# Performance work log

Measured on AMD Instinct MI355X. Metric: run time of the kernel, lower is better.

Reference implementation:

```python
import jax, jax.numpy as jnp
import numpy as np

# CODABlocks (codomain attention) with per_channel_attention=True:
# token_codimension = head_codimension = 1, scale = 2, n_modes = [32, 32],
# mixer_modes = [16, 16], temperature = 1.0, instance_norm (affine) everywhere.
N_HEADS = 16
TEMPERATURE = 1.0
EPS = 1e-5

def _gelu(z):
    return jax.nn.gelu(z, approximate=False)  # matches torch F.gelu default (erf)

def instance_norm(x, g, b):
    # x: (B, C, H, W); normalize over spatial dims per (sample, channel), affine.
    mu = jnp.mean(x, axis=(-2, -1), keepdims=True)
    var = jnp.var(x, axis=(-2, -1), keepdims=True)
    return (x - mu) * jax.lax.rsqrt(var + EPS) * g[:, None, None] + b[:, None, None]

def conv1x1(x, w, b):
    return jnp.einsum('bihw,io->bohw', x, w) + b[None, :, None, None]

def fourier_resample(x, out_shape):
    # FFT-based spatial resampling (mode truncation / zero-pad), norm='forward'.
    if tuple(x.shape[-2:]) == tuple(out_shape):
        return x
    Ho, Wo = out_shape
    xft = jnp.fft.rfftn(x, axes=(-2, -1), norm='forward')
    out = jnp.zeros(x.shape[:-2] + (Ho, Wo // 2 + 1), dtype=xft.dtype)
    hk = min(x.shape[-2], Ho) // 2
    wk = min(xft.shape[-1], Wo // 2 + 1)
    out = out.at[..., :hk, :wk].set(xft[..., :hk, :wk])
    out = out.at[..., -hk:, :wk].set(xft[..., -hk:, :wk])
    return jnp.fft.irfftn(out, s=out_shape, axes=(-2, -1), norm='forward')

def spectral_conv(x, w, out_shape):
    # Truncated-mode spectral convolution (dense weights, equiv. to tucker rank=1.0).
    # w: (Cin, Cout, 2*mh, mw, 2) -> complex weight on kept Fourier modes.
    wc = w[..., 0] + 1j * w[..., 1]
    mh = wc.shape[2] // 2
    mw = wc.shape[3]
    Ho, Wo = out_shape
    xft = jnp.fft.rfftn(x, axes=(-2, -1), norm='forward')   # (B, Cin, H, W//2+1)
    top = jnp.einsum('bihw,iohw->bohw', xft[:, :, :mh, :mw], wc[:, :, :mh])
    bot = jnp.einsum('bihw,iohw->bohw', xft[:, :, -mh:, :mw], wc[:, :, mh:])
    out_ft = jnp.zeros((x.shape[0], wc.shape[1], Ho, Wo // 2 + 1), dtype=xft.dtype)
    out_ft = out_ft.at[:, :, :mh, :mw].set(top)
    out_ft = out_ft.at[:, :, -mh:, :mw].set(bot)
    return jnp.fft.irfftn(out_ft, s=out_shape, axes=(-2, -1), norm='forward')

def fno_layer(x, spec_w, skip_w, skip_b, out_shape, norm=None, act=None):
    # One FNOBlocks layer: spectral conv + (resampled) linear skip, optional norm/act.
    xs = fourier_resample(conv1x1(x, skip_w, skip_b), out_shape)
    xf = spectral_conv(x, spec_w, out_shape)
    if norm is not None:
        xf = instance_norm(xf, *norm)
    y = xf + xs
    return act(y) if act is not None else y

def codano_forward(x, key_w, key_skip_w, key_skip_b, query_w, query_skip_w, query_skip_b, value_w, value_skip_w, value_skip_b, proj_w, proj_skip_w, proj_skip_b, norm1_g, norm1_b, attn_norm_g, attn_norm_b, norm2_g, norm2_b, mixer_w1, mixer_skip_w1, mixer_skip_b1, mixer_norm_g1, mixer_norm_b1, mixer_w2, mixer_skip_w2, mixer_skip_b2, mixer_norm_g2, mixer_norm_b2, mixer_out_g, mixer_out_b):
    b, t, H, W = x.shape   # token codim d = 1 -> channel dim == number of tokens
    tokens = x.reshape(b * t, 1, H, W)
    tokens_norm = instance_norm(tokens, norm1_g, norm1_b)
    Hs, Ws = H // 2, W // 2   # K, Q downsampled by scale = 2
    k = fno_layer(tokens_norm, key_w, key_skip_w, key_skip_b, (Hs, Ws))
    q = fno_layer(tokens_norm, query_w, query_skip_w, query_skip_b, (Hs, Ws))
    v = fno_layer(tokens_norm, value_w, value_skip_w, value_skip_b, (H, W))

    def heads_flat(z):
        hh, ww = z.shape[-2:]
        # (b*t, n_heads*d, h, w) -> (b, heads, t, d*h*w), d = 1
        return z.reshape(b, t, N_HEADS, hh * ww).transpose(0, 2, 1, 3)

    kf, qf, vf = heads_flat(k), heads_flat(q), heads_flat(v)
    scale = jnp.sqrt(jnp.asarray(kf.shape[-1], jnp.float32)) * TEMPERATURE
    dprod = jax.nn.softmax(jnp.einsum('bhtd,bhsd->bhts', qf, kf) / scale, axis=-1)
    attn = jnp.einsum('bhts,bhsd->bhtd', dprod, vf)      # (b, heads, t, H*W)
    attn = attn.transpose(0, 2, 1, 3).reshape(b * t, N_HEADS, H, W)
    # multi-head projection back to token codimension (n_heads -> 1)
    attn = fno_layer(attn, proj_w, proj_skip_w, proj_skip_b, (H, W))
    attn = instance_norm(attn + tokens, attn_norm_g, attn_norm_b)
    # permutation-equivariant mixer: 2 FNO layers shared across all tokens
    m = instance_norm(attn, norm2_g, norm2_b)
    m = fno_layer(m, mixer_w1, mixer_skip_w1, mixer_skip_b1, (H, W), norm=(mixer_norm_g1, mixer_norm_b1), act=_gelu)
    m = fno_layer(m, mixer_w2, mixer_skip_w2, mixer_skip_b2, (H, W), norm=(mixer_norm_g2, mixer_norm_b2))
    out = instance_norm(m, mixer_out_g, mixer_out_b) + attn
    return out.reshape(b, t, H, W)

def setup_inputs():
    key = jax.random.key(0)
    ks = list(jax.random.split(key, 32))
    f32 = jnp.float32
    def W_(k, shape, s=0.02):
        return (s * jax.random.normal(k, shape)).astype(f32)
    B, T, H, Wd = 4, 32, 128, 128
    mh_s, mw_s = 16, 9    # mixer_modes [16,16]: 2*(16//2) rows, 16//2+1 rfft cols
    mh_f, mw_f = 32, 17   # n_modes [32,32]
    return {
        'x': jax.random.normal(ks[0], (B, T, H, Wd), dtype=f32),
        'key_w': W_(ks[1], (1, N_HEADS, mh_s, mw_s, 2)),
        'key_skip_w': W_(ks[2], (1, N_HEADS), 0.5),
        'key_skip_b': W_(ks[3], (N_HEADS,)),
        'query_w': W_(ks[4], (1, N_HEADS, mh_s, mw_s, 2)),
        'query_skip_w': W_(ks[5], (1, N_HEADS), 0.5),
        'query_skip_b': W_(ks[6], (N_HEADS,)),
        'value_w': W_(ks[7], (1, N_HEADS, mh_s, mw_s, 2)),
        'value_skip_w': W_(ks[8], (1, N_HEADS), 0.5),
        'value_skip_b': W_(ks[9], (N_HEADS,)),
        'proj_w': W_(ks[10], (N_HEADS, 1, mh_f, mw_f, 2)),
        'proj_skip_w': W_(ks[11], (N_HEADS, 1), 0.25),
        'proj_skip_b': W_(ks[12], (1,)),
        'norm1_g': jnp.ones((1,), f32), 'norm1_b': jnp.zeros((1,), f32),
        'attn_norm_g': jnp.ones((1,), f32), 'attn_norm_b': jnp.zeros((1,), f32),
        'norm2_g': jnp.ones((1,), f32), 'norm2_b': jnp.zeros((1,), f32),
        'mixer_w1': W_(ks[13], (1, 1, mh_f, mw_f, 2)),
        'mixer_skip_w1': W_(ks[14], (1, 1), 0.5),
        'mixer_skip_b1': W_(ks[15], (1,)),
        'mixer_norm_g1': jnp.ones((1,), f32), 'mixer_norm_b1': jnp.zeros((1,), f32),
        'mixer_w2': W_(ks[16], (1, 1, mh_f, mw_f, 2)),
        'mixer_skip_w2': W_(ks[17], (1, 1), 0.5),
        'mixer_skip_b2': W_(ks[18], (1,)),
        'mixer_norm_g2': jnp.ones((1,), f32), 'mixer_norm_b2': jnp.zeros((1,), f32),
        'mixer_out_g': jnp.ones((1,), f32), 'mixer_out_b': jnp.zeros((1,), f32),
    }

def reference(x, key_w, key_skip_w, key_skip_b, query_w, query_skip_w, query_skip_b, value_w, value_skip_w, value_skip_b, proj_w, proj_skip_w, proj_skip_b, norm1_g, norm1_b, attn_norm_g, attn_norm_b, norm2_g, norm2_b, mixer_w1, mixer_skip_w1, mixer_skip_b1, mixer_norm_g1, mixer_norm_b1, mixer_w2, mixer_skip_w2, mixer_skip_b2, mixer_norm_g2, mixer_norm_b2, mixer_out_g, mixer_out_b):
    return codano_forward(x, key_w, key_skip_w, key_skip_b, query_w, query_skip_w, query_skip_b, value_w, value_skip_w, value_skip_b, proj_w, proj_skip_w, proj_skip_b, norm1_g, norm1_b, attn_norm_g, attn_norm_b, norm2_g, norm2_b, mixer_w1, mixer_skip_w1, mixer_skip_b1, mixer_norm_g1, mixer_norm_b1, mixer_w2, mixer_skip_w2, mixer_skip_b2, mixer_norm_g2, mixer_norm_b2, mixer_out_g, mixer_out_b)
```

## Files before the change

kernel.cpp:

```cpp
#include <hip/hip_runtime.h>
#include <cmath>

#define PI_F 3.14159265358979323846f
#define NTOK 128
#define NPIX 16384
#define NHEADS 16

__device__ __forceinline__ void block_reduce2(float& a, float& b){
  __shared__ float sa[4], sb[4];
  __syncthreads();
  for (int o=32;o>0;o>>=1){ a += __shfl_down(a,o); b += __shfl_down(b,o); }
  int w = threadIdx.x>>6, l = threadIdx.x&63;
  if (l==0){ sa[w]=a; sb[w]=b; }
  __syncthreads();
  a = sa[0]+sa[1]+sa[2]+sa[3];
  b = sb[0]+sb[1]+sb[2]+sb[3];
}

__device__ __forceinline__ float block_reduce1(float a){
  __shared__ float sa[4];
  __syncthreads();
  for (int o=32;o>0;o>>=1) a += __shfl_down(a,o);
  int w = threadIdx.x>>6, l = threadIdx.x&63;
  if (l==0) sa[w]=a;
  __syncthreads();
  return sa[0]+sa[1]+sa[2]+sa[3];
}

__device__ __forceinline__ float gelu_f(float y){
  return 0.5f*y*(1.f + erff(y*0.70710678118f));
}

__device__ __forceinline__ void affine_from(const float* __restrict__ ps, float g, float bb, int t,
                                            float& a, float& b0){
  float sum=0.f,sq=0.f;
  #pragma unroll
  for (int s=0;s<8;s++){ const float* p=ps+((size_t)t*8+s)*2; sum+=p[0]; sq+=p[1]; }
  const float iN=1.f/NPIX;
  float mu=sum*iN, var=sq*iN-mu*mu;
  a=rsqrtf(var+1e-5f)*g;
  b0=bb-mu*a;
}
__device__ __forceinline__ void scalA_from(const float* __restrict__ psA, float ag, float n2g, int t,
                                           float& muZ, float& aA, float& a0){
  float sum=0.f,sq=0.f;
  #pragma unroll
  for (int s=0;s<16;s++){ const float* p=psA+((size_t)t*16+s)*2; sum+=p[0]; sq+=p[1]; }
  const float iN=1.f/NPIX;
  muZ=sum*iN; float var=sq*iN-muZ*muZ;
  float inv=rsqrtf(var+1e-5f);
  aA=inv*ag;
  float var2=aA*aA*var;
  a0=aA*rsqrtf(var2+1e-5f)*n2g;
}
__device__ __forceinline__ void scalB_from(const float* __restrict__ psB, float mng1, int t,
                                           float& mu1, float& c1){
  float sum=0.f,sq=0.f;
  #pragma unroll
  for (int s=0;s<16;s++){ const float* p=psB+((size_t)t*16+s)*2; sum+=p[0]; sq+=p[1]; }
  const float iN=1.f/NPIX;
  mu1=sum*iN; float var=sq*iN-mu1*mu1;
  c1=rsqrtf(var+1e-5f)*mng1;
}
__device__ __forceinline__ void scalC_from(const float* __restrict__ psC, float mng2, float K, float sw,
                                           float outg, int t,
                                           float& mu2f, float& c2, float& mu3, float& c3){
  float sf=0.f,sfsq=0.f,sm=0.f,smsq=0.f,sx=0.f;
  #pragma unroll
  for (int s=0;s<16;s++){
    const float* p=psC+((size_t)t*16+s)*5;
    sf+=p[0]; sfsq+=p[1]; sm+=p[2]; smsq+=p[3]; sx+=p[4];
  }
  const float iN=1.f/NPIX;
  mu2f=sf*iN; float var2=sfsq*iN-mu2f*mu2f;
  c2=rsqrtf(var2+1e-5f)*mng2;
  float Em1=sm*iN, Em1sq=smsq*iN, Exm=sx*iN;
  float Em2=K+sw*Em1;
  float Em2sq = c2*c2*var2 + sw*sw*Em1sq + K*K
              + 2.f*c2*sw*(Exm - mu2f*Em1) + 2.f*K*sw*Em1;
  float var_m2=Em2sq-Em2*Em2;
  mu3=Em2;
  c3=rsqrtf(var_m2+1e-5f)*outg;
}

__global__ __launch_bounds__(256) void k_stats0(const float* __restrict__ x, float* __restrict__ pstat){
  int t=blockIdx.x, slab=blockIdx.y;
  const float* xs = x + (size_t)t*NPIX + slab*2048;
  float sum=0.f, sq=0.f;
  for (int i=threadIdx.x;i<2048;i+=256){ float v=xs[i]; sum+=v; sq+=v*v; }
  block_reduce2(sum,sq);
  if (threadIdx.x==0){ float* o=pstat+((size_t)t*8+slab)*2; o[0]=sum; o[1]=sq; }
}

__global__ __launch_bounds__(256) void k_colfft33(const float* __restrict__ x, const float* __restrict__ pstat0,
                          const float* __restrict__ n1g, const float* __restrict__ n1b,
                          float* __restrict__ A){
  __shared__ float rows[16*128];
  __shared__ float tw[128][2];
  int base = blockIdx.x*16;
  int t = base>>7;
  float a,b0; affine_from(pstat0, n1g[0], n1b[0], t, a, b0);
  for (int i=threadIdx.x;i<2048;i+=256) rows[i] = a*x[(size_t)base*128 + i] + b0;
  for (int p=threadIdx.x;p<128;p+=256){ float sn,cs; sincosf(-(2.f*PI_F/128.f)*(float)p,&sn,&cs); tw[p][0]=cs; tw[p][1]=sn; }
  __syncthreads();
  for (int e=threadIdx.x;e<16*33;e+=256){
    int r=e/33, c=e%33;
    const float* rp=rows+r*128;
    float re=0.f, im=0.f;
    for (int w=0;w<128;w++){
      int p=(c*w)&127;
      float v=rp[w];
      re+=v*tw[p][0]; im+=v*tw[p][1];
    }
    float* o=A+((size_t)(base+r)*33+c)*2; o[0]=re; o[1]=im;
  }
}

__global__ __launch_bounds__(256) void k_rowfft64(const float* __restrict__ A,
                          float* __restrict__ X64, float* __restrict__ X64h){
  int s=blockIdx.x, cg2=blockIdx.y;
  int c0=cg2*11;
  __shared__ float a[128][11][2];
  __shared__ float S[64][11][2];
  __shared__ float tw[128][2];
  for (int i=threadIdx.x;i<128*22;i+=256){
    int r=i/22, q=i%22;
    a[r][q>>1][q&1] = A[((size_t)(s*128+r)*33 + c0)*2 + q];
  }
  for (int p=threadIdx.x;p<128;p+=256){ float sn,cs; sincosf(-(2.f*PI_F/128.f)*(float)p,&sn,&cs); tw[p][0]=cs; tw[p][1]=sn; }
  __syncthreads();
  const float sc=1.f/16384.f;
  for (int e=threadIdx.x;e<64*11;e+=256){
    int i2=e/11, cl=e%11;
    int r=(i2<32)? i2 : i2+64;
    float re=0.f, im=0.f;
    for (int h=0;h<128;h++){
      int p=(r*h)&127;
      float cs=tw[p][0], sn=tw[p][1];
      float ar=a[h][cl][0], ai=a[h][cl][1];
      re+=ar*cs-ai*sn; im+=ar*sn+ai*cs;
    }
    S[i2][cl][0]=re*sc; S[i2][cl][1]=im*sc;
  }
  __syncthreads();
  for (int e=threadIdx.x;e<64*11;e+=256){
    int r=e/11, cl=e%11; int c=c0+cl;
    float vr=S[r][cl][0], vi=S[r][cl][1];
    float* o=X64+((size_t)s*(64*33)+r*33+c)*2; o[0]=vr; o[1]=vi;
    float hr=vr, hi=vi;
    if (c==0 || c==32){
      int pr=(64-r)&63;
      hr=0.5f*(vr+S[pr][cl][0]);
      hi=0.5f*(vi-S[pr][cl][1]);
    }
    float* oh=X64h+((size_t)s*(64*33)+r*33+c)*2; oh[0]=hr; oh[1]=hi;
  }
}

__global__ __launch_bounds__(256) void k_UeZYw(const float* __restrict__ X64, const float* __restrict__ X64h,
    const float* __restrict__ qw, const float* __restrict__ qsw,
    const float* __restrict__ kw, const float* __restrict__ ksw,
    const float* __restrict__ value_w, const float* __restrict__ vsw, const float* __restrict__ vsb,
    const float* __restrict__ proj_w, const float* __restrict__ psw,
    float* __restrict__ Zq, float* __restrict__ Zk, float* __restrict__ Yw,
    float* __restrict__ Ue){
  __shared__ float sh[4224];
  int bx=blockIdx.x;
  if (bx<2048){
    int t=bx>>4, h=bx&15;
    float* Xs = sh;
    float2* xh0 = (float2*)(sh+1092);
    for (int e=threadIdx.x;e<544;e+=256){
      int j=e/17, c=e%17;
      int i2=(j<16)? j : (j+32);
      const float* xp = X64 + ((size_t)t*(64*33) + i2*33 + c)*2;
      Xs[e*2]=xp[0]; Xs[e*2+1]=xp[1];
    }
    if (threadIdx.x<17){
      int j=threadIdx.x;
      int r=(j<=8)? j : j+47;
      const float* hp = X64h + ((size_t)t*(64*33) + r*33)*2;
      xh0[j]=make_float2(hp[0],hp[1]);
    }
    __syncthreads();
    float aq=qsw[h], ak=ksw[h];
    for (int e=threadIdx.x;e<306;e+=256){
      int side=e/153, m=e%153;
      int j=m/9, c=m%9;
      int jj=(j<=8)? j : j+15;
      const float* W = side? kw : qw;
      float a = side? ak : aq;
      float prx=0.f, pry=0.f;
      if (j!=8){
        int jw=(j<8)? j : j-1;
        const float* wp = W + ((size_t)(h*16+jw)*9 + c)*2;
        float xrr=Xs[(jj*17+c)*2], xri=Xs[(jj*17+c)*2+1];
        prx = wp[0]*xrr - wp[1]*xri;
        pry = wp[0]*xri + wp[1]*xrr;
      }
      float Vx=prx, Vy=pry;
      if (c==0){
        int jp = (j==0)? 0 : 17-j;
        float ppx=0.f, ppy=0.f;
        if (jp!=8){
          int jw2=(jp<8)? jp : jp-1;
          const float* wp2 = W + ((size_t)(h*16+jw2)*9)*2;
          int jj2=(jp<=8)? jp : jp+15;
          float x2r=Xs[(jj2*17)*2], x2i=Xs[(jj2*17)*2+1];
          ppx = wp2[0]*x2r - wp2[1]*x2i;
          ppy = wp2[0]*x2i + wp2[1]*x2r;
        }
        Vx = 0.5f*(prx + ppx);
        Vy = 0.5f*(pry - ppy);
      }
      float xmr, xmi;
      if (c==0){ xmr=xh0[j].x; xmi=xh0[j].y; }
      else { xmr=Xs[(jj*17+c)*2]; xmi=Xs[(jj*17+c)*2+1]; }
      float zr = a*xmr + Vx;
      float zi = a*xmi + Vy;
      float wf = (side && c!=0)? 2.f : 1.f;
      float* dst = (side? Zk : Zq) + ((size_t)(t*16+h))*306 + m*2;
      dst[0]=wf*zr; dst[1]=wf*zi;
    }
    int b=t>>5, s=t&31;
    float vw=vsw[h], vb=vsb[h], pw=psw[h];
    size_t obase = ((size_t)(b*16+h)*32 + s)*1088;
    for (int e=threadIdx.x;e<544;e+=256){
      int j=e/17, c=e%17;
      float xr=Xs[e*2], xi=Xs[e*2+1];
      float wvr=0.f,wvi=0.f;
      if (c<=8 && (j<8||j>=24)){
        int jw=(j<8)? j : (j-16);
        const float* wv = value_w + ((size_t)(h*16+jw)*9 + c)*2;
        wvr=wv[0]; wvi=wv[1];
      }
      float Mr=xr*wvr-xi*wvi, Mi=xr*wvi+xi*wvr;
      float Mhr=Mr, Mhi=Mi;
      if (c==0){
        float Pr2=0.f,Pi2=0.f;
        int jp2=(j==0)?0:((j==16)?-1:32-j);
        if (jp2>=0 && (jp2<8||jp2>=24)){
          int jw2=(jp2<8)? jp2 : (jp2-16);
          const float* wv2=value_w+((size_t)(h*16+jw2)*9)*2;
          float pxr=Xs[(jp2*17)*2], pxi=Xs[(jp2*17)*2+1];
          Pr2=pxr*wv2[0]-pxi*wv2[1];
          Pi2=pxr*wv2[1]+pxi*wv2[0];
        }
        Mhr=0.5f*(Mr+Pr2); Mhi=0.5f*(Mi-Pi2);
      }
      float Yr=vw*xr+Mhr+((e==0)? vb:0.f);
      float Yi=vw*xi+Mhi;
      const float* pc=proj_w+((size_t)(h*32+j)*17+c)*2;
      float pr=pc[0], pi=pc[1];
      float* o=Yw+obase+e*2;
      o[0]=pr*Yr-pi*Yi+pw*Mr;
      o[1]=pr*Yi+pi*Yr+pw*Mi;
    }
  } else {
    int u=bx-2048;
    int b=u>>8, rem=u&255, t=rem>>3, sg=rem&7;
    float2* xt=(float2*)sh;
    const float2* src = (const float2*)(X64h + ((size_t)(b*32+t))*4224);
    for (int m=threadIdx.x;m<2112;m+=256){
      int r=m/33, c=m%33;
      bool excl = (c<=8) && (r<=8 || r>=56);
      float w = excl? 0.f : ((c==0||c==32)? 1.f : 2.f);
      float2 v = src[m];
      xt[m]=make_float2(v.x*w, v.y*w);
    }
    __syncthreads();
    float acc[4]={0.f,0.f,0.f,0.f};
    const float2* s0=(const float2*)(X64h + ((size_t)(b*32+sg*4))*4224);
    for (int m=threadIdx.x;m<2112;m+=256){
      float2 a2=xt[m];
      #pragma unroll
      for (int j=0;j<4;j++){
        float2 b2=s0[(size_t)j*2112+m];
        acc[j]+=a2.x*b2.x+a2.y*b2.y;
      }
    }
    for (int j=0;j<4;j++){
      float r=block_reduce1(acc[j]);
      if (threadIdx.x==0) Ue[((size_t)(b*32+t))*32 + sg*4+j]=r;
    }
  }
}

__global__ __launch_bounds__(256) void k_scores2(const float* __restrict__ Zq, const float* __restrict__ Zk,
                          const float* __restrict__ Ue,
                          const float* __restrict__ qsw, const float* __restrict__ qsb,
                          const float* __restrict__ ksw, const float* __restrict__ ksb,
                          float* __restrict__ P){
  int b=blockIdx.x, h=blockIdx.y, tz=blockIdx.z;
  __shared__ float2 zq[16][154];
  __shared__ float2 zk[16][154];
  __shared__ float Pl[16][33];
  for (int i=threadIdx.x;i<16*153;i+=256){
    int t=i/153, m=i%153;
    zq[t][m]=((const float2*)(Zq + ((size_t)((b*32+tz*16+t)*16+h))*306))[m];
  }
  float aq=qsw[h], ak=ksw[h], bq=qsb[h], bk=ksb[h];
  float aqak=aq*ak;
  int tl=threadIdx.x>>4, sl=threadIdx.x&15;
  for (int ch=0; ch<2; ch++){
    __syncthreads();
    for (int i=threadIdx.x;i<16*153;i+=256){
      int s=i/153, m=i%153;
      zk[s][m]=((const float2*)(Zk + ((size_t)((b*32+ch*16+s)*16+h))*306))[m];
    }
    __syncthreads();
    float acc=0.f;
    for (int m=0;m<153;m++){
      float2 a2=zq[tl][m], c2=zk[sl][m];
      acc += a2.x*c2.x + a2.y*c2.y;
    }
    int s=ch*16+sl;
    float G = aqak*Ue[((size_t)(b*32+tz*16+tl))*32+s] + acc;
    Pl[tl][s] = 64.f*(G + bk*zq[tl][0].x + bq*zk[sl][0].x + bq*bk);
  }
  __syncthreads();
  if (threadIdx.x<16){
    int tt=threadIdx.x;
    float mx=-INFINITY;
    for (int s=0;s<32;s++) mx=fmaxf(mx,Pl[tt][s]);
    float e[32]; float sum=0.f;
    for (int s=0;s<32;s++){ e[s]=expf(Pl[tt][s]-mx); sum+=e[s]; }
    float inv=1.f/sum;
    size_t base=((size_t)(b*16+h)*32+tz*16+tt)*32;
    for (int s=0;s<32;s++) P[base+s]=e[s]*inv;
  }
}

__global__ __launch_bounds__(256) void k_SfSk(const float* __restrict__ x, const float* __restrict__ P,
        const float* __restrict__ Yw,
        const float* __restrict__ pw, const float* __restrict__ vw,
        const float* __restrict__ pstat0, const float* __restrict__ n1g, const float* __restrict__ n1b,
        float* __restrict__ Sfp, float* __restrict__ sk){
  __shared__ float sh[4096];
  int bx=blockIdx.x;
  if (bx<272){
    int b=bx/68, rem=bx%68, ec=rem/4, g=rem%4;
    int e0=ec*64, hs0=g*128;
    float (*Pl)[32] = (float(*)[32])sh;
    for (int i=threadIdx.x;i<128*32;i+=256){
      int hsl=i>>5, t=i&31;
      int hs=hs0+hsl, h=hs>>5, s=hs&31;
      Pl[hsl][t]=P[(((size_t)(b*16+h)*32)+t)*32+s];
    }
    __syncthreads();
    int el=threadIdx.x&63, tg=threadIdx.x>>6;
    float acc[8];
    #pragma unroll
    for (int j=0;j<8;j++) acc[j]=0.f;
    const float* Yb = Yw + ((size_t)b*512 + hs0)*1088 + e0 + el;
    #pragma unroll 4
    for (int hsl=0;hsl<128;hsl++){
      float y = Yb[(size_t)hsl*1088];
      #pragma unroll
      for (int j=0;j<8;j++) acc[j] += Pl[hsl][tg*8+j]*y;
    }
    #pragma unroll
    for (int j=0;j<8;j++){
      int t=tg*8+j;
      Sfp[((size_t)(b*32+t)*4+g)*1088 + e0 + el] = acc[j];
    }
  } else {
    int u=bx-272;
    int b=u>>6, rem=u&63, ch=rem>>1, tt=rem&1;
    int pxb=ch*512;
    float* Rs = sh;
    float* cbs = sh+512;
    float* as2 = sh+528;
    float* b0s = sh+560;
    if (threadIdx.x<32){
      float a,b0; affine_from(pstat0, n1g[0], n1b[0], b*32+threadIdx.x, a, b0);
      as2[threadIdx.x]=a; b0s[threadIdx.x]=b0;
    }
    __syncthreads();
    for (int rr=threadIdx.x; rr<512; rr+=256){
      int tl=rr>>5, s=rr&31;
      int t=tt*16+tl;
      float acc=0.f;
      for (int h=0;h<16;h++)
        acc += pw[h]*vw[h]*P[(((size_t)(b*16+h)*32)+t)*32+s];
      Rs[tl*32+s]=acc*as2[s];
      float cb=acc*b0s[s];
      for (int o=16;o>0;o>>=1) cb+=__shfl_down(cb,o,32);
      if (s==0) cbs[tl]=cb;
    }
    __syncthreads();
    float a0[16], a1[16];
    #pragma unroll
    for (int t=0;t<16;t++){ a0[t]=0.f; a1[t]=0.f; }
    for (int s=0;s<32;s++){
      const float* xp = x + ((size_t)(b*32+s))*NPIX + pxb;
      float v0=xp[threadIdx.x], v1=xp[threadIdx.x+256];
      #pragma unroll
      for (int t=0;t<16;t++){ float r=Rs[t*32+s]; a0[t]+=r*v0; a1[t]+=r*v1; }
    }
    #pragma unroll
    for (int t=0;t<16;t++){
      int gt=tt*16+t;
      float cb=cbs[t];
      float* op = sk + ((size_t)(b*32+gt))*NPIX + pxb;
      op[threadIdx.x]=a0[t]+cb; op[threadIdx.x+256]=a1[t]+cb;
    }
  }
}

__global__ __launch_bounds__(256) void k_field0(const float* __restrict__ Sfp,
        const float* __restrict__ sk, const float* __restrict__ x,
        const float* __restrict__ psw, const float* __restrict__ vsb, const float* __restrict__ psb,
        float* __restrict__ zf, float* __restrict__ pstatA){
  int bt = blockIdx.x, slab = blockIdx.y;
  __shared__ float Ss[1088];
  __shared__ float T[8*17*2];
  __shared__ float tw[128][2];
  for (int i=threadIdx.x;i<1088;i+=256){
    const float* sp4 = Sfp + (size_t)bt*4352 + i;
    Ss[i] = sp4[0]+sp4[1088]+sp4[2176]+sp4[3264];
  }
  for (int p=threadIdx.x;p<128;p+=256){ float sn,cs; sincosf((2.f*PI_F/128.f)*(float)p,&sn,&cs); tw[p][0]=cs; tw[p][1]=sn; }
  __syncthreads();
  int h0 = slab*8;
  for (int e=threadIdx.x;e<8*17;e+=256){
    int hl=e/17, c=e%17; int h=h0+hl;
    float re=0.f, im=0.f;
    for (int j=0;j<32;j++){
      int r=(j<16)? j : (j+96);
      int p=(r*h)&127;
      float cs=tw[p][0], sn=tw[p][1];
      float ar=Ss[(j*17+c)*2], ai=Ss[(j*17+c)*2+1];
      re += ar*cs - ai*sn;
      im += ar*sn + ai*cs;
    }
    T[e*2]=re; T[e*2+1]=im;
  }
  __syncthreads();
  size_t base = (size_t)bt*NPIX + h0*128;
  float Cb = psb[0];
  for (int hh=0;hh<16;hh++) Cb += psw[hh]*vsb[hh];
  float sum=0.f, sq=0.f;
  for (int pos=threadIdx.x;pos<1024;pos+=256){
    int hl=pos>>7, w=pos&127;
    const float* Th=T+hl*17*2;
    float br=tw[w][0], bi=tw[w][1];
    float rr=br, ri=bi;
    float v=Th[0];
    for (int c=1;c<17;c++){
      v += 2.f*(Th[c*2]*rr - Th[c*2+1]*ri);
      float nr=rr*br-ri*bi; ri=rr*bi+ri*br; rr=nr;
    }
    float val = v + sk[base+pos] + x[base+pos] + Cb;
    zf[base+pos]=val; sum+=val; sq+=val*val;
  }
  block_reduce2(sum,sq);
  if (threadIdx.x==0){ float* o=pstatA+((size_t)bt*16+slab)*2; o[0]=sum; o[1]=sq; }
}

__global__ __launch_bounds__(256) void k_specm0(const float* __restrict__ P,
    const float* __restrict__ pw, const float* __restrict__ vw,
    const float* __restrict__ Sfp, const float* __restrict__ X64,
    const float* __restrict__ pstat0, const float* __restrict__ pstatA,
    const float* __restrict__ n1g, const float* __restrict__ n1b,
    const float* __restrict__ ag, const float* __restrict__ n2g, const float* __restrict__ n2b,
    const float* __restrict__ psw, const float* __restrict__ vsb, const float* __restrict__ psb,
    float* __restrict__ sp){
  int bt=blockIdx.x, ec=blockIdx.y; int b=bt>>5, t=bt&31;
  __shared__ float Rs[32];
  __shared__ float Sfl[1088];
  if (threadIdx.x<32){
    int s=threadIdx.x; float acc=0.f;
    for (int h=0;h<16;h++)
      acc += pw[h]*vw[h]*P[(((size_t)(b*16+h)*32)+t)*32+s];
    Rs[s]=acc;
  }
  for (int i=threadIdx.x;i<1088;i+=256){
    const float* sp4 = Sfp + (size_t)bt*4352 + i;
    Sfl[i]=sp4[0]+sp4[1088]+sp4[2176]+sp4[3264];
  }
  __syncthreads();
  float a_t,b0_t; affine_from(pstat0,n1g[0],n1b[0],bt,a_t,b0_t);
  float muZ,aA,a0; scalA_from(pstatA,ag[0],n2g[0],bt,muZ,aA,a0);
  float Cb=psb[0];
  for (int h=0;h<16;h++) Cb+=psw[h]*vsb[h];
  float inva=1.f/a_t;
  int e1=ec*272, e2=e1+272;
  for (int e=e1+threadIdx.x;e<e2;e+=256){
    int j=e/17, c=e%17;
    float sr=Sfl[e*2], si=Sfl[e*2+1];
    if (c==0){
      if (j==0){ si=0.f; }
      else if (j==16){ sr*=0.5f; si*=0.5f; }
      else { int jp=32-j; sr=0.5f*(sr+Sfl[jp*34]); si=0.5f*(si-Sfl[jp*34+1]); }
    }
    int i2=(j<16)? j : (j+32);
    float re=0.f, im=0.f;
    const float* xb = X64 + ((size_t)(b*32)*(64*33) + i2*33 + c)*2;
    for (int s=0;s<32;s++){
      const float* xp = xb + (size_t)s*(64*33)*2;
      float r=Rs[s];
      re += r*xp[0]; im += r*xp[1];
    }
    const float* xt = X64 + ((size_t)bt*(64*33) + i2*33 + c)*2;
    re += inva*xt[0]; im += inva*xt[1];
    float zr=sr+re, zi=si+im;
    if (e==0) zr += Cb - b0_t*inva;
    float mr=a0*zr, mi=a0*zi;
    if (e==0) mr += n2b[0] - muZ*a0;
    sp[((size_t)bt*544+e)*2]=mr; sp[((size_t)bt*544+e)*2+1]=mi;
  }
}

__global__ __launch_bounds__(256) void k_field1(const float* __restrict__ sp, const float* __restrict__ wm,
        float* __restrict__ fd1, float* __restrict__ pstatB){
  int bt = blockIdx.x, slab = blockIdx.y;
  __shared__ float Ss[1088];
  __shared__ float T[8*17*2];
  __shared__ float tw[128][2];
  for (int e=threadIdx.x;e<544;e+=256){
    float xr=sp[((size_t)bt*544+e)*2], xi=sp[((size_t)bt*544+e)*2+1];
    float wr=wm[e*2], wi=wm[e*2+1];
    Ss[e*2]=xr*wr-xi*wi; Ss[e*2+1]=xr*wi+xi*wr;
  }
  for (int p=threadIdx.x;p<128;p+=256){ float sn,cs; sincosf((2.f*PI_F/128.f)*(float)p,&sn,&cs); tw[p][0]=cs; tw[p][1]=sn; }
  __syncthreads();
  int h0 = slab*8;
  for (int e=threadIdx.x;e<8*17;e+=256){
    int hl=e/17, c=e%17; int h=h0+hl;
    float re=0.f, im=0.f;
    for (int j=0;j<32;j++){
      int r=(j<16)? j : (j+96);
      int p=(r*h)&127;
      float cs=tw[p][0], sn=tw[p][1];
      float ar=Ss[(j*17+c)*2], ai=Ss[(j*17+c)*2+1];
      re += ar*cs - ai*sn;
      im += ar*sn + ai*cs;
    }
    T[e*2]=re; T[e*2+1]=im;
  }
  __syncthreads();
  size_t base = (size_t)bt*NPIX + h0*128;
  float sum=0.f, sq=0.f;
  for (int pos=threadIdx.x;pos<1024;pos+=256){
    int hl=pos>>7, w=pos&127;
    const float* Th=T+hl*17*2;
    float br=tw[w][0], bi=tw[w][1];
    float rr=br, ri=bi;
    float v=Th[0];
    for (int c=1;c<17;c++){
      v += 2.f*(Th[c*2]*rr - Th[c*2+1]*ri);
      float nr=rr*br-ri*bi; ri=rr*bi+ri*br; rr=nr;
    }
    fd1[base+pos]=v; sum+=v; sq+=v*v;
  }
  block_reduce2(sum,sq);
  if (threadIdx.x==0){ float* o=pstatB+((size_t)bt*16+slab)*2; o[0]=sum; o[1]=sq; }
}

__global__ __launch_bounds__(256) void k_colA1(const float* __restrict__ f1, const float* __restrict__ z,
        const float* __restrict__ pstatA, const float* __restrict__ pstatB,
        const float* __restrict__ ag, const float* __restrict__ n2g, const float* __restrict__ mng1,
        const float* __restrict__ n2b,
        const float* __restrict__ mnb1, const float* __restrict__ msw1, const float* __restrict__ msb1,
        float* __restrict__ A){
  __shared__ float rows[16*128];
  __shared__ float tw[128][2];
  int grow = blockIdx.x*16;
  int t = grow>>7;
  float muZ,aA,a0;
  scalA_from(pstatA, ag[0], n2g[0], t, muZ, aA, a0);
  float b2 = n2b[0];
  float mu1,c1;
  scalB_from(pstatB, mng1[0], t, mu1, c1);
  float nb=mnb1[0], sw=msw1[0], sb=msb1[0];
  for (int i=threadIdx.x;i<2048;i+=256){
    size_t gi=(size_t)grow*128+i;
    float m0v=(z[gi]-muZ)*a0+b2;
    float y=(f1[gi]-mu1)*c1+nb + m0v*sw + sb;
    rows[i]=gelu_f(y);
  }
  for (int p=threadIdx.x;p<128;p+=256){ float sn,cs; sincosf(-(2.f*PI_F/128.f)*(float)p,&sn,&cs); tw[p][0]=cs; tw[p][1]=sn; }
  __syncthreads();
  for (int e=threadIdx.x;e<16*17;e+=256){
    int r=e/17, c=e%17;
    const float* rp=rows+r*128;
    float re=0.f, im=0.f;
    for (int w=0;w<128;w++){
      int p=(c*w)&127;
      float v=rp[w];
      re+=v*tw[p][0]; im+=v*tw[p][1];
    }
    float* o=A+((size_t)(grow+r)*17+c)*2; o[0]=re; o[1]=im;
  }
}

__global__ __launch_bounds__(256) void k_rowfft32(const float* __restrict__ A, float* __restrict__ spec){
  int s=blockIdx.x, cg2=blockIdx.y;
  int c0 = (cg2==0)? 0 : (1+cg2*4);
  int nc = (cg2==0)? 5 : 4;
  __shared__ float a[128*5*2];
  __shared__ float tw[128][2];
  for (int i=threadIdx.x;i<128*nc*2;i+=256){
    int r=i/(2*nc), q=i%(2*nc);
    a[(r*5+(q>>1))*2+(q&1)] = A[((size_t)(s*128+r)*17 + c0)*2 + q];
  }
  for (int p=threadIdx.x;p<128;p+=256){ float sn,cs; sincosf(-(2.f*PI_F/128.f)*(float)p,&sn,&cs); tw[p][0]=cs; tw[p][1]=sn; }
  __syncthreads();
  const float sc=1.f/16384.f;
  for (int e=threadIdx.x;e<32*nc;e+=256){
    int j=e/nc, cl=e%nc;
    int r=(j<16)? j : (j+96);
    float re=0.f,im=0.f;
    for (int h=0;h<128;h++){
      int p=(r*h)&127;
      float cs=tw[p][0], sn=tw[p][1];
      float ar=a[(h*5+cl)*2], ai=a[(h*5+cl)*2+1];
      re += ar*cs - ai*sn;
      im += ar*sn + ai*cs;
    }
    float* o=spec+((size_t)s*544 + j*17 + c0+cl)*2;
    o[0]=re*sc; o[1]=im*sc;
  }
}

__global__ __launch_bounds__(256) void k_field2(const float* __restrict__ sp2, const float* __restrict__ wm,
        const float* __restrict__ f1, const float* __restrict__ z,
        const float* __restrict__ pstatA, const float* __restrict__ pstatB,
        const float* __restrict__ ag, const float* __restrict__ n2g, const float* __restrict__ mng1,
        const float* __restrict__ n2b, const float* __restrict__ mnb1,
        const float* __restrict__ msw1, const float* __restrict__ msb1,
        float* __restrict__ fd2, float* __restrict__ pstatC){
  int bt = blockIdx.x, slab = blockIdx.y;
  __shared__ float Ss[1088];
  __shared__ float T[8*17*2];
  __shared__ float tw[128][2];
  for (int e=threadIdx.x;e<544;e+=256){
    float xr=sp2[((size_t)bt*544+e)*2], xi=sp2[((size_t)bt*544+e)*2+1];
    float wr=wm[e*2], wi=wm[e*2+1];
    Ss[e*2]=xr*wr-xi*wi; Ss[e*2+1]=xr*wi+xi*wr;
  }
  for (int p=threadIdx.x;p<128;p+=256){ float sn,cs; sincosf((2.f*PI_F/128.f)*(float)p,&sn,&cs); tw[p][0]=cs; tw[p][1]=sn; }
  __syncthreads();
  int h0 = slab*8;
  for (int e=threadIdx.x;e<8*17;e+=256){
    int hl=e/17, c=e%17; int h=h0+hl;
    float re=0.f, im=0.f;
    for (int j=0;j<32;j++){
      int r=(j<16)? j : (j+96);
      int p=(r*h)&127;
      float cs=tw[p][0], sn=tw[p][1];
      float ar=Ss[(j*17+c)*2], ai=Ss[(j*17+c)*2+1];
      re += ar*cs - ai*sn;
      im += ar*sn + ai*cs;
    }
    T[e*2]=re; T[e*2+1]=im;
  }
  __syncthreads();
  size_t base = (size_t)bt*NPIX + h0*128;
  float muZ,aA,a0,mu1,c1;
  scalA_from(pstatA, ag[0], n2g[0], bt, muZ, aA, a0);
  scalB_from(pstatB, mng1[0], bt, mu1, c1);
  float b2=n2b[0], nb1=mnb1[0], sw1=msw1[0], sb1=msb1[0];
  float s_f=0.f,s_fsq=0.f,s_m=0.f,s_msq=0.f,s_x=0.f;
  for (int pos=threadIdx.x;pos<1024;pos+=256){
    int hl=pos>>7, w=pos&127;
    const float* Th=T+hl*17*2;
    float br=tw[w][0], bi=tw[w][1];
    float rr=br, ri=bi;
    float v=Th[0];
    for (int c=1;c<17;c++){
      v += 2.f*(Th[c*2]*rr - Th[c*2+1]*ri);
      float nr=rr*br-ri*bi; ri=rr*bi+ri*br; rr=nr;
    }
    size_t gi=base+pos;
    float m0v=(z[gi]-muZ)*a0+b2;
    float y=(f1[gi]-mu1)*c1+nb1 + m0v*sw1 + sb1;
    float m1v=gelu_f(y);
    fd2[gi]=v;
    s_f+=v; s_fsq+=v*v; s_m+=m1v; s_msq+=m1v*m1v; s_x+=v*m1v;
  }
  block_reduce2(s_f,s_fsq);
  block_reduce2(s_m,s_msq);
  s_x = block_reduce1(s_x);
  if (threadIdx.x==0){
    float* o=pstatC+((size_t)bt*16+slab)*5;
    o[0]=s_f; o[1]=s_fsq; o[2]=s_m; o[3]=s_msq; o[4]=s_x;
  }
}

__global__ __launch_bounds__(256) void k_final2(const float* __restrict__ z, const float* __restrict__ f1,
        const float* __restrict__ f2,
        const float* __restrict__ pstatA, const float* __restrict__ pstatB, const float* __restrict__ pstatC,
        const float* __restrict__ ag, const float* __restrict__ n2g, const float* __restrict__ mng1,
        const float* __restrict__ mng2, const float* __restrict__ outg,
        const float* __restrict__ ab, const float* __restrict__ n2b,
        const float* __restrict__ mnb1, const float* __restrict__ msw1, const float* __restrict__ msb1,
        const float* __restrict__ mnb2, const float* __restrict__ msw2, const float* __restrict__ msb2,
        const float* __restrict__ outb, float* __restrict__ out){
  int bt=blockIdx.x, slab=blockIdx.y;
  float muZ,aA,a0,mu1,c1,mu2f,c2,mu3,c3;
  scalA_from(pstatA, ag[0], n2g[0], bt, muZ, aA, a0);
  scalB_from(pstatB, mng1[0], bt, mu1, c1);
  float sw2=msw2[0], K=mnb2[0]+msb2[0];
  scalC_from(pstatC, mng2[0], K, sw2, outg[0], bt, mu2f, c2, mu3, c3);
  float b1=ab[0], b2=n2b[0], nb1=mnb1[0], sw1=msw1[0], sb1=msb1[0];
  float nb2=mnb2[0], sb2=msb2[0], bo=outb[0];
  size_t base=(size_t)bt*NPIX + (size_t)slab*1024;
  for (int i=threadIdx.x;i<1024;i+=256){
    size_t gi=base+i;
    float zv=z[gi];
    float m0v=(zv-muZ)*a0+b2;
    float a2v=(zv-muZ)*aA+b1;
    float y=(f1[gi]-mu1)*c1+nb1 + m0v*sw1 + sb1;
    float m1v=gelu_f(y);
    float m2v=(f2[gi]-mu2f)*c2+nb2 + m1v*sw2 + sb2;
    out[gi]=(m2v-mu3)*c3+bo+a2v;
  }
}

extern "C" void kernel_launch(void* const* d_in, const int* in_sizes, int n_in,
                              void* d_out, int out_size, void* d_ws, size_t ws_size,
                              hipStream_t stream){
  const float* x        = (const float*)d_in[0];
  const float* key_w    = (const float*)d_in[1];
  const float* key_sw   = (const float*)d_in[2];
  const float* key_sb   = (const float*)d_in[3];
  const float* query_w  = (const float*)d_in[4];
  const float* query_sw = (const float*)d_in[5];
  const float* query_sb = (const float*)d_in[6];
  const float* value_w  = (const float*)d_in[7];
  const float* value_sw = (const float*)d_in[8];
  const float* value_sb = (const float*)d_in[9];
  const float* proj_w   = (const float*)d_in[10];
  const float* proj_sw  = (const float*)d_in[11];
  const float* proj_sb  = (const float*)d_in[12];
  const float* norm1_g  = (const float*)d_in[13];
  const float* norm1_b  = (const float*)d_in[14];
  const float* attn_g   = (const float*)d_in[15];
  const float* attn_b   = (const float*)d_in[16];
  const float* norm2_g  = (const float*)d_in[17];
  const float* norm2_b  = (const float*)d_in[18];
  const float* mw1      = (const float*)d_in[19];
  const float* msw1     = (const float*)d_in[20];
  const float* msb1     = (const float*)d_in[21];
  const float* mng1     = (const float*)d_in[22];
  const float* mnb1     = (const float*)d_in[23];
  const float* mw2      = (const float*)d_in[24];
  const float* msw2     = (const float*)d_in[25];
  const float* msb2     = (const float*)d_in[26];
  const float* mng2     = (const float*)d_in[27];
  const float* mnb2     = (const float*)d_in[28];
  const float* outg     = (const float*)d_in[29];
  const float* outb     = (const float*)d_in[30];
  float* out = (float*)d_out;
  float* ws  = (float*)d_ws;

  size_t off=0;
  float* A   = ws + off; off += (size_t)128*128*33*2;
  float* X64 = ws + off; off += (size_t)128*64*33*2;
  float* X64h= ws + off; off += (size_t)128*64*33*2;
  float* Zq  = ws + off; off += (size_t)128*16*306;
  float* Zk  = ws + off; off += (size_t)128*16*306;
  float* Ue  = ws + off; off += (size_t)4*32*32;
  float* P   = ws + off; off += (size_t)4*16*32*32;
  float* Yw  = ws + off; off += (size_t)2048*1088;
  float* Sfp = ws + off; off += (size_t)128*4*1088;
  float* sk  = ws + off; off += (size_t)128*16384;
  float* zf  = ws + off; off += (size_t)128*16384;
  float* fd1 = ws + off; off += (size_t)128*16384;
  float* fd2 = ws + off; off += (size_t)128*16384;
  float* sp  = ws + off; off += (size_t)128*544*2;
  float* sp2 = ws + off; off += (size_t)128*544*2;
  float* pstat0 = ws + off; off += (size_t)128*8*2;
  float* pstatA = ws + off; off += (size_t)128*16*2;
  float* pstatB = ws + off; off += (size_t)128*16*2;
  float* pstatC = ws + off; off += (size_t)128*16*5;

  k_stats0<<<dim3(128,8),256,0,stream>>>(x, pstat0);
  k_colfft33<<<1024,256,0,stream>>>(x, pstat0, norm1_g, norm1_b, A);
  k_rowfft64<<<dim3(128,3),256,0,stream>>>(A, X64, X64h);
  k_UeZYw<<<3072,256,0,stream>>>(X64, X64h, query_w, query_sw, key_w, key_sw,
      value_w, value_sw, value_sb, proj_w, proj_sw, Zq, Zk, Yw, Ue);
  k_scores2<<<dim3(4,16,2),256,0,stream>>>(Zq, Zk, Ue, query_sw, query_sb, key_sw, key_sb, P);
  k_SfSk<<<528,256,0,stream>>>(x, P, Yw, proj_sw, value_sw, pstat0, norm1_g, norm1_b, Sfp, sk);

  k_field0<<<dim3(128,16),256,0,stream>>>(Sfp, sk, x, proj_sw, value_sb, proj_sb, zf, pstatA);
  k_specm0<<<dim3(128,2),256,0,stream>>>(P, proj_sw, value_sw, Sfp, X64, pstat0, pstatA,
      norm1_g, norm1_b, attn_g, norm2_g, norm2_b, proj_sw, value_sb, proj_sb, sp);
  k_field1<<<dim3(128,16),256,0,stream>>>(sp, mw1, fd1, pstatB);
  k_colA1<<<1024,256,0,stream>>>(fd1, zf, pstatA, pstatB, attn_g, norm2_g, mng1,
      norm2_b, mnb1, msw1, msb1, A);
  k_rowfft32<<<dim3(128,4),256,0,stream>>>(A, sp2);
  k_field2<<<dim3(128,16),256,0,stream>>>(sp2, mw2, fd1, zf, pstatA, pstatB,
      attn_g, norm2_g, mng1, norm2_b, mnb1, msw1, msb1, fd2, pstatC);
  k_final2<<<dim3(128,16),256,0,stream>>>(zf, fd1, fd2, pstatA, pstatB, pstatC,
      attn_g, norm2_g, mng1, mng2, outg, attn_b, norm2_b,
      mnb1, msw1, msb1, mnb2, msw2, msb2, outb, out);
}
```

Measured before the change: 304.8 us.

## Merge independent kernels via block-index dispatch and defer norm affine to spectral domain

Input statistics and the column DFT now run in one launch, split by block index. The instance-norm affine is applied afterwards in the row FFT as a scale plus a DC offset, which linearity of the DFT allows. The field0 and specm0 kernels are merged into one launch with disjoint block ranges. The attention-norm scaling moves from specm0 into field1, so specm0 no longer depends on the field0 statistics. The aim is fewer launches and less serialization on the stream, at the cost of extra per-block branching and a shared-memory size fixed at the larger of the two paths.

Measured after the change: 301.9 us. About the same (-1.0%).

```diff
diff --git a/kernel.cpp b/kernel.cpp
--- a/kernel.cpp
+++ b/kernel.cpp
@@ -83,40 +83,41 @@
   c3=rsqrtf(var_m2+1e-5f)*outg;
 }
 
-__global__ __launch_bounds__(256) void k_stats0(const float* __restrict__ x, float* __restrict__ pstat){
-  int t=blockIdx.x, slab=blockIdx.y;
-  const float* xs = x + (size_t)t*NPIX + slab*2048;
-  float sum=0.f, sq=0.f;
-  for (int i=threadIdx.x;i<2048;i+=256){ float v=xs[i]; sum+=v; sq+=v*v; }
-  block_reduce2(sum,sq);
-  if (threadIdx.x==0){ float* o=pstat+((size_t)t*8+slab)*2; o[0]=sum; o[1]=sq; }
-}
-
-__global__ __launch_bounds__(256) void k_colfft33(const float* __restrict__ x, const float* __restrict__ pstat0,
+__global__ __launch_bounds__(256) void k_scol(const float* __restrict__ x,
+                        float* __restrict__ A, float* __restrict__ pstat){
+  __shared__ float sh[2304];
+  int bx=blockIdx.x;
+  if (bx<1024){
+    float* rows = sh;
+    float* tw = sh+2048;
+    int base = bx*16;
+    for (int i=threadIdx.x;i<2048;i+=256) rows[i] = x[(size_t)base*128 + i];
+    for (int p=threadIdx.x;p<128;p+=256){ float sn,cs; sincosf(-(2.f*PI_F/128.f)*(float)p,&sn,&cs); tw[p*2]=cs; tw[p*2+1]=sn; }
+    __syncthreads();
+    for (int e=threadIdx.x;e<16*33;e+=256){
+      int r=e/33, c=e%33;
+      const float* rp=rows+r*128;
+      float re=0.f, im=0.f;
+      for (int w=0;w<128;w++){
+        int p=(c*w)&127;
+        float v=rp[w];
+        re+=v*tw[p*2]; im+=v*tw[p*2+1];
+      }
+      float* o=A+((size_t)(base+r)*33+c)*2; o[0]=re; o[1]=im;
+    }
+  } else {
+    int u=bx-1024; int t=u>>3, slab=u&7;
+    const float* xs = x + (size_t)t*NPIX + slab*2048;
+    float sum=0.f, sq=0.f;
+    for (int i=threadIdx.x;i<2048;i+=256){ float v=xs[i]; sum+=v; sq+=v*v; }
+    block_reduce2(sum,sq);
+    if (threadIdx.x==0){ float* o=pstat+((size_t)t*8+slab)*2; o[0]=sum; o[1]=sq; }
+  }
+}
+
+__global__ __launch_bounds__(256) void k_rowfft64(const float* __restrict__ A,
+                          const float* __restrict__ pstat0,
                           const float* __restrict__ n1g, const float* __restrict__ n1b,
-                          float* __restrict__ A){
-  __shared__ float rows[16*128];
-  __shared__ float tw[128][2];
-  int base = blockIdx.x*16;
-  int t = base>>7;
-  float a,b0; affine_from(pstat0, n1g[0], n1b[0], t, a, b0);
-  for (int i=threadIdx.x;i<2048;i+=256) rows[i] = a*x[(size_t)base*128 + i] + b0;
-  for (int p=threadIdx.x;p<128;p+=256){ float sn,cs; sincosf(-(2.f*PI_F/128.f)*(float)p,&sn,&cs); tw[p][0]=cs; tw[p][1]=sn; }
-  __syncthreads();
-  for (int e=threadIdx.x;e<16*33;e+=256){
-    int r=e/33, c=e%33;
-    const float* rp=rows+r*128;
-    float re=0.f, im=0.f;
-    for (int w=0;w<128;w++){
-      int p=(c*w)&127;
-      float v=rp[w];
-      re+=v*tw[p][0]; im+=v*tw[p][1];
-    }
-    float* o=A+((size_t)(base+r)*33+c)*2; o[0]=re; o[1]=im;
-  }
-}
-
-__global__ __launch_bounds__(256) void k_rowfft64(const float* __restrict__ A,
                           float* __restrict__ X64, float* __restrict__ X64h){
   int s=blockIdx.x, cg2=blockIdx.y;
   int c0=cg2*11;
@@ -128,6 +129,7 @@
     a[r][q>>1][q&1] = A[((size_t)(s*128+r)*33 + c0)*2 + q];
   }
   for (int p=threadIdx.x;p<128;p+=256){ float sn,cs; sincosf(-(2.f*PI_F/128.f)*(float)p,&sn,&cs); tw[p][0]=cs; tw[p][1]=sn; }
+  float af,b0; affine_from(pstat0, n1g[0], n1b[0], s, af, b0);
   __syncthreads();
   const float sc=1.f/16384.f;
   for (int e=threadIdx.x;e<64*11;e+=256){
@@ -140,7 +142,9 @@
       float ar=a[h][cl][0], ai=a[h][cl][1];
       re+=ar*cs-ai*sn; im+=ar*sn+ai*cs;
     }
-    S[i2][cl][0]=re*sc; S[i2][cl][1]=im*sc;
+    float vr = af*re*sc, vi = af*im*sc;
+    if (r==0 && (c0+cl)==0) vr += b0;
+    S[i2][cl][0]=vr; S[i2][cl][1]=vi;
   }
   __syncthreads();
   for (int e=threadIdx.x;e<64*11;e+=256){
@@ -408,118 +412,118 @@
   }
 }
 
-__global__ __launch_bounds__(256) void k_field0(const float* __restrict__ Sfp,
+__global__ __launch_bounds__(256) void k_f0sp(const float* __restrict__ Sfp,
         const float* __restrict__ sk, const float* __restrict__ x,
+        const float* __restrict__ P, const float* __restrict__ X64,
+        const float* __restrict__ pstat0,
+        const float* __restrict__ n1g, const float* __restrict__ n1b,
+        const float* __restrict__ pw, const float* __restrict__ vw,
         const float* __restrict__ psw, const float* __restrict__ vsb, const float* __restrict__ psb,
-        float* __restrict__ zf, float* __restrict__ pstatA){
-  int bt = blockIdx.x, slab = blockIdx.y;
-  __shared__ float Ss[1088];
-  __shared__ float T[8*17*2];
-  __shared__ float tw[128][2];
-  for (int i=threadIdx.x;i<1088;i+=256){
-    const float* sp4 = Sfp + (size_t)bt*4352 + i;
-    Ss[i] = sp4[0]+sp4[1088]+sp4[2176]+sp4[3264];
-  }
-  for (int p=threadIdx.x;p<128;p+=256){ float sn,cs; sincosf((2.f*PI_F/128.f)*(float)p,&sn,&cs); tw[p][0]=cs; tw[p][1]=sn; }
-  __syncthreads();
-  int h0 = slab*8;
-  for (int e=threadIdx.x;e<8*17;e+=256){
-    int hl=e/17, c=e%17; int h=h0+hl;
-    float re=0.f, im=0.f;
-    for (int j=0;j<32;j++){
-      int r=(j<16)? j : (j+96);
-      int p=(r*h)&127;
-      float cs=tw[p][0], sn=tw[p][1];
-      float ar=Ss[(j*17+c)*2], ai=Ss[(j*17+c)*2+1];
-      re += ar*cs - ai*sn;
-      im += ar*sn + ai*cs;
-    }
-    T[e*2]=re; T[e*2+1]=im;
-  }
-  __syncthreads();
-  size_t base = (size_t)bt*NPIX + h0*128;
-  float Cb = psb[0];
-  for (int hh=0;hh<16;hh++) Cb += psw[hh]*vsb[hh];
-  float sum=0.f, sq=0.f;
-  for (int pos=threadIdx.x;pos<1024;pos+=256){
-    int hl=pos>>7, w=pos&127;
-    const float* Th=T+hl*17*2;
-    float br=tw[w][0], bi=tw[w][1];
-    float rr=br, ri=bi;
-    float v=Th[0];
-    for (int c=1;c<17;c++){
-      v += 2.f*(Th[c*2]*rr - Th[c*2+1]*ri);
-      float nr=rr*br-ri*bi; ri=rr*bi+ri*br; rr=nr;
-    }
-    float val = v + sk[base+pos] + x[base+pos] + Cb;
-    zf[base+pos]=val; sum+=val; sq+=val*val;
-  }
-  block_reduce2(sum,sq);
-  if (threadIdx.x==0){ float* o=pstatA+((size_t)bt*16+slab)*2; o[0]=sum; o[1]=sq; }
-}
-
-__global__ __launch_bounds__(256) void k_specm0(const float* __restrict__ P,
-    const float* __restrict__ pw, const float* __restrict__ vw,
-    const float* __restrict__ Sfp, const float* __restrict__ X64,
-    const float* __restrict__ pstat0, const float* __restrict__ pstatA,
-    const float* __restrict__ n1g, const float* __restrict__ n1b,
-    const float* __restrict__ ag, const float* __restrict__ n2g, const float* __restrict__ n2b,
-    const float* __restrict__ psw, const float* __restrict__ vsb, const float* __restrict__ psb,
-    float* __restrict__ sp){
-  int bt=blockIdx.x, ec=blockIdx.y; int b=bt>>5, t=bt&31;
-  __shared__ float Rs[32];
-  __shared__ float Sfl[1088];
-  if (threadIdx.x<32){
-    int s=threadIdx.x; float acc=0.f;
-    for (int h=0;h<16;h++)
-      acc += pw[h]*vw[h]*P[(((size_t)(b*16+h)*32)+t)*32+s];
-    Rs[s]=acc;
-  }
-  for (int i=threadIdx.x;i<1088;i+=256){
-    const float* sp4 = Sfp + (size_t)bt*4352 + i;
-    Sfl[i]=sp4[0]+sp4[1088]+sp4[2176]+sp4[3264];
-  }
-  __syncthreads();
-  float a_t,b0_t; affine_from(pstat0,n1g[0],n1b[0],bt,a_t,b0_t);
-  float muZ,aA,a0; scalA_from(pstatA,ag[0],n2g[0],bt,muZ,aA,a0);
-  float Cb=psb[0];
-  for (int h=0;h<16;h++) Cb+=psw[h]*vsb[h];
-  float inva=1.f/a_t;
-  int e1=ec*272, e2=e1+272;
-  for (int e=e1+threadIdx.x;e<e2;e+=256){
-    int j=e/17, c=e%17;
-    float sr=Sfl[e*2], si=Sfl[e*2+1];
-    if (c==0){
-      if (j==0){ si=0.f; }
-      else if (j==16){ sr*=0.5f; si*=0.5f; }
-      else { int jp=32-j; sr=0.5f*(sr+Sfl[jp*34]); si=0.5f*(si-Sfl[jp*34+1]); }
-    }
-    int i2=(j<16)? j : (j+32);
-    float re=0.f, im=0.f;
-    const float* xb = X64 + ((size_t)(b*32)*(64*33) + i2*33 + c)*2;
-    for (int s=0;s<32;s++){
-      const float* xp = xb + (size_t)s*(64*33)*2;
-      float r=Rs[s];
-      re += r*xp[0]; im += r*xp[1];
-    }
-    const float* xt = X64 + ((size_t)bt*(64*33) + i2*33 + c)*2;
-    re += inva*xt[0]; im += inva*xt[1];
-    float zr=sr+re, zi=si+im;
-    if (e==0) zr += Cb - b0_t*inva;
-    float mr=a0*zr, mi=a0*zi;
-    if (e==0) mr += n2b[0] - muZ*a0;
-    sp[((size_t)bt*544+e)*2]=mr; sp[((size_t)bt*544+e)*2+1]=mi;
+        float* __restrict__ zf, float* __restrict__ pstatA, float* __restrict__ sp){
+  __shared__ float sh[1616];
+  int bx=blockIdx.x;
+  if (bx<2048){
+    int bt=bx>>4, slab=bx&15;
+    float* Ss=sh; float* T=sh+1088; float* tw=sh+1360;
+    for (int i=threadIdx.x;i<1088;i+=256){
+      const float* sp4 = Sfp + (size_t)bt*4352 + i;
+      Ss[i] = sp4[0]+sp4[1088]+sp4[2176]+sp4[3264];
+    }
+    for (int p=threadIdx.x;p<128;p+=256){ float sn,cs; sincosf((2.f*PI_F/128.f)*(float)p,&sn,&cs); tw[p*2]=cs; tw[p*2+1]=sn; }
+    __syncthreads();
+    int h0 = slab*8;
+    for (int e=threadIdx.x;e<136;e+=256){
+      int hl=e/17, c=e%17; int h=h0+hl;
+      float re=0.f, im=0.f;
+      for (int j=0;j<32;j++){
+        int r=(j<16)? j : (j+96);
+        int p=(r*h)&127;
+        float cs=tw[p*2], sn=tw[p*2+1];
+        float ar=Ss[(j*17+c)*2], ai=Ss[(j*17+c)*2+1];
+        re += ar*cs - ai*sn;
+        im += ar*sn + ai*cs;
+      }
+      T[e*2]=re; T[e*2+1]=im;
+    }
+    __syncthreads();
+    size_t base = (size_t)bt*NPIX + h0*128;
+    float Cb = psb[0];
+    for (int hh=0;hh<16;hh++) Cb += psw[hh]*vsb[hh];
+    float sum=0.f, sq=0.f;
+    for (int pos=threadIdx.x;pos<1024;pos+=256){
+      int hl=pos>>7, w=pos&127;
+      const float* Th=T+hl*17*2;
+      float br=tw[w*2], bi=tw[w*2+1];
+      float rr=br, ri=bi;
+      float v=Th[0];
+      for (int c=1;c<17;c++){
+        v += 2.f*(Th[c*2]*rr - Th[c*2+1]*ri);
+        float nr=rr*br-ri*bi; ri=rr*bi+ri*br; rr=nr;
+      }
+      float val = v + sk[base+pos] + x[base+pos] + Cb;
+      zf[base+pos]=val; sum+=val; sq+=val*val;
+    }
+    block_reduce2(sum,sq);
+    if (threadIdx.x==0){ float* o=pstatA+((size_t)bt*16+slab)*2; o[0]=sum; o[1]=sq; }
+  } else {
+    int u=bx-2048;
+    int bt=u>>1, ec=u&1; int b=bt>>5, t=bt&31;
+    float* Sfl=sh; float* Rs=sh+1088;
+    if (threadIdx.x<32){
+      int s=threadIdx.x; float acc=0.f;
+      for (int h=0;h<16;h++)
+        acc += pw[h]*vw[h]*P[(((size_t)(b*16+h)*32)+t)*32+s];
+      Rs[s]=acc;
+    }
+    for (int i=threadIdx.x;i<1088;i+=256){
+      const float* sp4 = Sfp + (size_t)bt*4352 + i;
+      Sfl[i]=sp4[0]+sp4[1088]+sp4[2176]+sp4[3264];
+    }
+    __syncthreads();
+    float a_t,b0_t; affine_from(pstat0,n1g[0],n1b[0],bt,a_t,b0_t);
+    float Cb=psb[0];
+    for (int h=0;h<16;h++) Cb+=psw[h]*vsb[h];
+    float inva=1.f/a_t;
+    int e1=ec*272, e2=e1+272;
+    for (int e=e1+threadIdx.x;e<e2;e+=256){
+      int j=e/17, c=e%17;
+      float sr=Sfl[e*2], si=Sfl[e*2+1];
+      if (c==0){
+        if (j==0){ si=0.f; }
+        else if (j==16){ sr*=0.5f; si*=0.5f; }
+        else { int jp=32-j; sr=0.5f*(sr+Sfl[jp*34]); si=0.5f*(si-Sfl[jp*34+1]); }
+      }
+      int i2=(j<16)? j : (j+32);
+      float re=0.f, im=0.f;
+      const float* xb = X64 + ((size_t)(b*32)*(64*33) + i2*33 + c)*2;
+      for (int s=0;s<32;s++){
+        const float* xp = xb + (size_t)s*(64*33)*2;
+        float r=Rs[s];
+        re += r*xp[0]; im += r*xp[1];
+      }
+      const float* xt = X64 + ((size_t)bt*(64*33) + i2*33 + c)*2;
+      re += inva*xt[0]; im += inva*xt[1];
+      float zr=sr+re, zi=si+im;
+      if (e==0) zr += Cb - b0_t*inva;
+      sp[((size_t)bt*544+e)*2]=zr; sp[((size_t)bt*544+e)*2+1]=zi;
+    }
   }
 }
 
 __global__ __launch_bounds__(256) void k_field1(const float* __restrict__ sp, const float* __restrict__ wm,
+        const float* __restrict__ pstatA,
+        const float* __restrict__ ag, const float* __restrict__ n2g, const float* __restrict__ n2b,
         float* __restrict__ fd1, float* __restrict__ pstatB){
   int bt = blockIdx.x, slab = blockIdx.y;
   __shared__ float Ss[1088];
   __shared__ float T[8*17*2];
   __shared__ float tw[128][2];
+  float muZ,aA,a0;
+  scalA_from(pstatA, ag[0], n2g[0], bt, muZ, aA, a0);
+  float d0 = n2b[0] - muZ*a0;
   for (int e=threadIdx.x;e<544;e+=256){
-    float xr=sp[((size_t)bt*544+e)*2], xi=sp[((size_t)bt*544+e)*2+1];
+    float xr=a0*sp[((size_t)bt*544+e)*2] + ((e==0)? d0 : 0.f);
+    float xi=a0*sp[((size_t)bt*544+e)*2+1];
     float wr=wm[e*2], wi=wm[e*2+1];
     Ss[e*2]=xr*wr-xi*wi; Ss[e*2+1]=xr*wi+xi*wr;
   }
@@ -777,18 +781,15 @@
   float* pstatB = ws + off; off += (size_t)128*16*2;
   float* pstatC = ws + off; off += (size_t)128*16*5;
 
-  k_stats0<<<dim3(128,8),256,0,stream>>>(x, pstat0);
-  k_colfft33<<<1024,256,0,stream>>>(x, pstat0, norm1_g, norm1_b, A);
-  k_rowfft64<<<dim3(128,3),256,0,stream>>>(A, X64, X64h);
+  k_scol<<<2048,256,0,stream>>>(x, A, pstat0);
+  k_rowfft64<<<dim3(128,3),256,0,stream>>>(A, pstat0, norm1_g, norm1_b, X64, X64h);
   k_UeZYw<<<3072,256,0,stream>>>(X64, X64h, query_w, query_sw, key_w, key_sw,
       value_w, value_sw, value_sb, proj_w, proj_sw, Zq, Zk, Yw, Ue);
   k_scores2<<<dim3(4,16,2),256,0,stream>>>(Zq, Zk, Ue, query_sw, query_sb, key_sw, key_sb, P);
   k_SfSk<<<528,256,0,stream>>>(x, P, Yw, proj_sw, value_sw, pstat0, norm1_g, norm1_b, Sfp, sk);
-
-  k_field0<<<dim3(128,16),256,0,stream>>>(Sfp, sk, x, proj_sw, value_sb, proj_sb, zf, pstatA);
-  k_specm0<<<dim3(128,2),256,0,stream>>>(P, proj_sw, value_sw, Sfp, X64, pstat0, pstatA,
-      norm1_g, norm1_b, attn_g, norm2_g, norm2_b, proj_sw, value_sb, proj_sb, sp);
-  k_field1<<<dim3(128,16),256,0,stream>>>(sp, mw1, fd1, pstatB);
+  k_f0sp<<<2304,256,0,stream>>>(Sfp, sk, x, P, X64, pstat0, norm1_g, norm1_b,
+      proj_sw, value_sw, proj_sw, value_sb, proj_sb, zf, pstatA, sp);
+  k_field1<<<dim3(128,16),256,0,stream>>>(sp, mw1, pstatA, attn_g, norm2_g, norm2_b, fd1, pstatB);
   k_colA1<<<1024,256,0,stream>>>(fd1, zf, pstatA, pstatB, attn_g, norm2_g, mng1,
       norm2_b, mnb1, msw1, msb1, A);
   k_rowfft32<<<dim3(128,4),256,0,stream>>>(A, sp2);
```
